# Kernel tuning notes

Measured on AMD Instinct MI355X. Metric: run time of the kernel, lower is better.

## Reference

```python
import jax, jax.numpy as jnp
import numpy as np

MAX_BITS = 64
HID = 768
B = 32768


def setup_inputs() -> dict:
    key = jax.random.key(0)
    ks = jax.random.split(key, 16)
    s = 0.02

    def w(k, shape):
        return jax.random.normal(k, shape, jnp.float32) * s

    a_bits = jnp.round(jax.random.uniform(ks[0], (B, MAX_BITS))).astype(jnp.float32)
    shift_amount = jax.random.randint(ks[1], (B,), 0, MAX_BITS).astype(jnp.int32)
    return {
        "a_bits": a_bits,
        "shift_amount": shift_amount,
        # shift_decoder: 64 -> 768 -> 768 -> 64 (weights stored [in, out])
        "Ws0": w(ks[2], (MAX_BITS, HID)), "bs0": jnp.zeros((HID,), jnp.float32),
        "Ws1": w(ks[3], (HID, HID)),      "bs1": jnp.zeros((HID,), jnp.float32),
        "Ws2": w(ks[4], (HID, MAX_BITS)), "bs2": jnp.zeros((MAX_BITS,), jnp.float32),
        # index_net: 128 -> 768 -> 768 -> 64
        "Wi0": w(ks[5], (2 * MAX_BITS, HID)), "bi0": jnp.zeros((HID,), jnp.float32),
        "Wi1": w(ks[6], (HID, HID)),          "bi1": jnp.zeros((HID,), jnp.float32),
        "Wi2": w(ks[7], (HID, MAX_BITS)),     "bi2": jnp.zeros((MAX_BITS,), jnp.float32),
        # validity_net: 128 -> 384 -> 1
        "Wv0": w(ks[8], (2 * MAX_BITS, HID // 2)), "bv0": jnp.zeros((HID // 2,), jnp.float32),
        "Wv1": w(ks[9], (HID // 2, 1)),            "bv1": jnp.zeros((1,), jnp.float32),
    }


def reference(a_bits, shift_amount, Ws0, bs0, Ws1, bs1, Ws2, bs2,
              Wi0, bi0, Wi1, bi1, Wi2, bi2, Wv0, bv0, Wv1, bv1):
    bits = a_bits.shape[1]  # == MAX_BITS == 64
    # decompose integer shift into bits: [B, bits]
    shift_bits = ((shift_amount[:, None] >> jnp.arange(bits, dtype=shift_amount.dtype)) & 1).astype(jnp.float32)
    # shift_decoder MLP -> hard one-hot of predicted shift
    h = jax.nn.relu(shift_bits @ Ws0 + bs0)
    h = jax.nn.relu(h @ Ws1 + bs1)
    shift_logits = (h @ Ws2 + bs2)[:, :bits]
    shift_soft = jax.nn.one_hot(jnp.argmax(shift_logits, axis=-1), bits, dtype=jnp.float32)  # [B, bits]
    # combined = [out_pos(one_hot(i)), shift_soft]; out_pos contribution to layer-0 is just row i of the
    # first `bits` rows of the weight, so precompute the shift_soft part once.
    base_i = shift_soft @ Wi0[bits:] + bi0   # [B, HID]
    base_v = shift_soft @ Wv0[bits:] + bv0   # [B, HID//2]

    def step(carry, i):
        h1 = jax.nn.relu(base_i + Wi0[i])                 # [B, HID]
        h2 = jax.nn.relu(h1 @ Wi1 + bi1)                  # [B, HID]
        idx_logits = (h2 @ Wi2 + bi2)[:, :bits]           # [B, bits]
        idx_soft = jax.nn.one_hot(jnp.argmax(idx_logits, axis=-1), bits, dtype=jnp.float32)
        pointed = jnp.sum(idx_soft * a_bits, axis=1)      # [B] soft gather
        hv = jax.nn.relu(base_v + Wv0[i])                 # [B, HID//2]
        valid = (hv @ Wv1 + bv1)[:, 0]                    # [B]
        return carry, pointed * jax.nn.sigmoid(valid)

    _, outs = jax.lax.scan(step, None, jnp.arange(bits))  # [bits, B]
    return outs.T                                          # [B, bits]
```

## Files before the change

kernel.cpp:

```cpp
#include <hip/hip_runtime.h>
#include <math.h>

#define HID 768
#define NB  64
#define HV  384

__device__ __forceinline__ float4 ld4(const float* p) { return *(const float4*)p; }

__global__ __launch_bounds__(256)
void dec1p_kernel(const float* __restrict__ Ws0, const float* __restrict__ bs0,
                  const float* __restrict__ Ws1, float* __restrict__ H1p) {
    __shared__ float W0s[7 * 48];
    __shared__ float As[48 * 68];
    __shared__ float Bs[48 * 68];
    const int tid = threadIdx.x;
    const int n0 = (blockIdx.x % 12) * 64;
    const int kz = blockIdx.x / 12;
    const int ks = kz * 48;

    for (int e = tid; e < 7 * 48; e += 256) {
        const int r = e / 48, c = e % 48;
        W0s[e] = (r < 6) ? Ws0[(size_t)r * HID + ks + c] : bs0[ks + c];
    }
    for (int e = tid; e < 48 * 16; e += 256) {
        const int k = e >> 4, nq = (e & 15) * 4;
        *(float4*)&Bs[k * 68 + nq] = ld4(Ws1 + (size_t)(ks + k) * HID + n0 + nq);
    }
    __syncthreads();
    for (int e = tid; e < 48 * 64; e += 256) {
        const int k = e >> 6, t = e & 63;
        float v = W0s[6 * 48 + k];
        #pragma unroll
        for (int b = 0; b < 6; ++b)
            v = fmaf((float)((t >> b) & 1), W0s[b * 48 + k], v);
        As[k * 68 + t] = fmaxf(v, 0.f);
    }
    __syncthreads();

    const int tx = tid & 15, ty = tid >> 4;
    float acc[4][4] = {};
    #pragma unroll 8
    for (int kk = 0; kk < 48; ++kk) {
        const float4 a4 = *(const float4*)&As[kk * 68 + ty * 4];
        const float4 b4 = *(const float4*)&Bs[kk * 68 + tx * 4];
        const float av[4] = {a4.x, a4.y, a4.z, a4.w};
        const float bv[4] = {b4.x, b4.y, b4.z, b4.w};
        #pragma unroll
        for (int a = 0; a < 4; ++a)
            #pragma unroll
            for (int b = 0; b < 4; ++b)
                acc[a][b] = fmaf(av[a], bv[b], acc[a][b]);
    }
    #pragma unroll
    for (int a = 0; a < 4; ++a) {
        float4 o = make_float4(acc[a][0], acc[a][1], acc[a][2], acc[a][3]);
        *(float4*)&H1p[((size_t)kz * 64 + ty * 4 + a) * HID + n0 + tx * 4] = o;
    }
}

__global__ __launch_bounds__(256)
void dec2_kernel(const float* __restrict__ H1p, const float* __restrict__ bs1,
                 const float* __restrict__ Ws2, const float* __restrict__ bs2,
                 int* __restrict__ pred) {
    __shared__ float sh[4 * HID];
    __shared__ float plp[4][4][64];
    __shared__ float lg[4][68];
    const int tid = threadIdx.x;
    const int t0 = blockIdx.x * 4;

    for (int e = tid; e < 4 * (HID / 4); e += 256) {
        const int rr = e / 192, k4 = (e % 192) * 4;
        float4 v = ld4(bs1 + k4);
        #pragma unroll
        for (int z = 0; z < 16; ++z) {
            const float4 p = ld4(H1p + ((size_t)z * 64 + t0 + rr) * HID + k4);
            v.x += p.x; v.y += p.y; v.z += p.z; v.w += p.w;
        }
        sh[rr * HID + k4 + 0] = fmaxf(v.x, 0.f);
        sh[rr * HID + k4 + 1] = fmaxf(v.y, 0.f);
        sh[rr * HID + k4 + 2] = fmaxf(v.z, 0.f);
        sh[rr * HID + k4 + 3] = fmaxf(v.w, 0.f);
    }
    __syncthreads();
    {
        const int n = tid & 63, part = tid >> 6;
        float p[4] = {0.f, 0.f, 0.f, 0.f};
        #pragma unroll 8
        for (int kk = 0; kk < 192; ++kk) {
            const int k = part * 192 + kk;
            const float w = Ws2[k * 64 + n];
            #pragma unroll
            for (int rr = 0; rr < 4; ++rr) p[rr] = fmaf(sh[rr * HID + k], w, p[rr]);
        }
        #pragma unroll
        for (int rr = 0; rr < 4; ++rr) plp[part][rr][n] = p[rr];
    }
    __syncthreads();
    {
        const int rr = tid >> 6, n = tid & 63;
        lg[rr][n] = bs2[n] + plp[0][rr][n] + plp[1][rr][n] + plp[2][rr][n] + plp[3][rr][n];
    }
    __syncthreads();
    if (tid < 4) {
        int best = 0; float bv = lg[tid][0];
        for (int n = 1; n < 64; ++n) {
            const float x = lg[tid][n];
            if (x > bv) { bv = x; best = n; }
        }
        pred[t0 + tid] = best;
    }
}

__global__ __launch_bounds__(64)
void plan_kernel(const int* __restrict__ pred, int* __restrict__ hdr) {
    const int lane = threadIdx.x;
    __shared__ int present[64];
    present[lane] = 0;
    __syncthreads();
    present[pred[lane] & 63] = 1;
    __syncthreads();
    const unsigned long long alive = __ballot(present[lane] != 0);
    const int P = __popcll(alive);
    const int rank = __popcll(alive & ((1ull << lane) - 1ull));
    if (lane == 0) hdr[0] = P;
    if (present[lane]) { hdr[1 + rank] = lane; hdr[65 + lane] = rank; }
    else hdr[65 + lane] = -1;
}

__global__ __launch_bounds__(256)
void gemmA_kernel(const float* __restrict__ Wi0, const float* __restrict__ bi0,
                  const float* __restrict__ Wi1, const int* __restrict__ hdr,
                  float* __restrict__ H2p) {
    __shared__ float As[64 * 68];
    __shared__ float Bs[64 * 40];
    const int tid = threadIdx.x;
    const int P = hdr[0];
    const int li = blockIdx.y;
    if (li >= P) return;
    const int s = hdr[1 + li];
    const int n0 = blockIdx.x * 32;
    const int z = blockIdx.z;
    const int tx = tid & 15, ty = tid >> 4;
    const float* arow = Wi0 + (size_t)(64 + s) * HID;
    float acc[4][2] = {};

    for (int kt = 0; kt < 2; ++kt) {
        const int k0 = z * 128 + kt * 64;
        #pragma unroll
        for (int pass = 0; pass < 4; ++pass) {
            const int c = pass * 256 + tid;
            const int m = c >> 4, kq = (c & 15) * 4;
            const float4 a1 = ld4(arow + k0 + kq);
            const float4 a2 = ld4(Wi0 + (size_t)m * HID + k0 + kq);
            const float4 bb = ld4(bi0 + k0 + kq);
            As[(kq + 0) * 68 + m] = fmaxf(a1.x + a2.x + bb.x, 0.f);
            As[(kq + 1) * 68 + m] = fmaxf(a1.y + a2.y + bb.y, 0.f);
            As[(kq + 2) * 68 + m] = fmaxf(a1.z + a2.z + bb.z, 0.f);
            As[(kq + 3) * 68 + m] = fmaxf(a1.w + a2.w + bb.w, 0.f);
        }
        #pragma unroll
        for (int pass = 0; pass < 2; ++pass) {
            const int c = pass * 256 + tid;
            const int k = c >> 3, nq = (c & 7) * 4;
            *(float4*)&Bs[k * 40 + nq] = ld4(Wi1 + (size_t)(k0 + k) * HID + n0 + nq);
        }
        __syncthreads();
        #pragma unroll 16
        for (int kk = 0; kk < 64; ++kk) {
            const float4 a4 = *(const float4*)&As[kk * 68 + ty * 4];
            const float2 b2 = *(const float2*)&Bs[kk * 40 + tx * 2];
            const float av[4] = {a4.x, a4.y, a4.z, a4.w};
            #pragma unroll
            for (int a = 0; a < 4; ++a) {
                acc[a][0] = fmaf(av[a], b2.x, acc[a][0]);
                acc[a][1] = fmaf(av[a], b2.y, acc[a][1]);
            }
        }
        __syncthreads();
    }
    float* dst = H2p + ((size_t)(z * 64 + li) * 64) * HID + n0 + tx * 2;
    #pragma unroll
    for (int a = 0; a < 4; ++a)
        *(float2*)(dst + (size_t)(ty * 4 + a) * HID) = make_float2(acc[a][0], acc[a][1]);
}

__global__ __launch_bounds__(256)
void gemmB_kernel(const float* __restrict__ bi1, const float* __restrict__ Wi2,
                  const int* __restrict__ hdr, const float* __restrict__ H2p,
                  float* __restrict__ PLf) {
    __shared__ float Ht[64 * 68];
    __shared__ float W2[64 * 68];
    const int tid = threadIdx.x;
    const int P = hdr[0];
    const int li = blockIdx.y;
    if (li >= P) return;
    const int bx = blockIdx.x;
    const int n0 = bx * 64;
    const size_t zstep = (size_t)64 * 64 * HID;

    for (int e = tid; e < 1024; e += 256) {
        const int m = e >> 4, nq = (e & 15) * 4;
        const float* base = H2p + ((size_t)li * 64 + m) * HID + n0 + nq;
        float4 v = ld4(base);
        #pragma unroll
        for (int z = 1; z < 6; ++z) {
            const float4 p = ld4(base + z * zstep);
            v.x += p.x; v.y += p.y; v.z += p.z; v.w += p.w;
        }
        const float4 bb = ld4(bi1 + n0 + nq);
        Ht[(nq + 0) * 68 + m] = fmaxf(v.x + bb.x, 0.f);
        Ht[(nq + 1) * 68 + m] = fmaxf(v.y + bb.y, 0.f);
        Ht[(nq + 2) * 68 + m] = fmaxf(v.z + bb.z, 0.f);
        Ht[(nq + 3) * 68 + m] = fmaxf(v.w + bb.w, 0.f);
    }
    #pragma unroll
    for (int pass = 0; pass < 4; ++pass) {
        const int c = pass * 256 + tid;
        const int cl = c >> 4, oq = (c & 15) * 4;
        *(float4*)&W2[cl * 68 + oq] = ld4(Wi2 + (size_t)(n0 + cl) * 64 + oq);
    }
    __syncthreads();
    const int tx = tid & 15, ty = tid >> 4;
    float pl_[4][4] = {};
    #pragma unroll 16
    for (int kk = 0; kk < 64; ++kk) {
        const float4 a4 = *(const float4*)&Ht[kk * 68 + ty * 4];
        const float4 b4 = *(const float4*)&W2[kk * 68 + tx * 4];
        const float av[4] = {a4.x, a4.y, a4.z, a4.w};
        const float bv[4] = {b4.x, b4.y, b4.z, b4.w};
        #pragma unroll
        for (int a = 0; a < 4; ++a)
            #pragma unroll
            for (int b = 0; b < 4; ++b)
                pl_[a][b] = fmaf(av[a], bv[b], pl_[a][b]);
    }
    #pragma unroll
    for (int a = 0; a < 4; ++a) {
        float4 o = make_float4(pl_[a][0], pl_[a][1], pl_[a][2], pl_[a][3]);
        *(float4*)&PLf[((size_t)(bx * 64 + li) * 64 + ty * 4 + a) * 64 + tx * 4] = o;
    }
}

__global__ __launch_bounds__(256)
void reduceA_kernel(const float* __restrict__ PLf, const float* __restrict__ bi2,
                    const float* __restrict__ Wv0, const float* __restrict__ bv0,
                    const float* __restrict__ Wv1, const float* __restrict__ bv1,
                    const int* __restrict__ hdr,
                    int* __restrict__ j_tab, float* __restrict__ sig_tab) {
    __shared__ float lg[16 * 68];
    const int tid = threadIdx.x;
    const int s = blockIdx.x >> 2;
    const int li = hdr[65 + s];
    if (li < 0) return;
    const int r0 = blockIdx.x * 16;
    const int rr = tid >> 4, q = tid & 15;
    const int i = (r0 & 63) + rr;
    float4 v = ld4(bi2 + q * 4);
    #pragma unroll
    for (int bx = 0; bx < 12; ++bx) {
        const float4 p = ld4(PLf + ((size_t)(bx * 64 + li) * 64 + i) * 64 + q * 4);
        v.x += p.x; v.y += p.y; v.z += p.z; v.w += p.w;
    }
    *(float4*)&lg[rr * 68 + q * 4] = v;
    __syncthreads();
    if (tid < 16) {
        int best = 0; float bv = lg[tid * 68];
        for (int n = 1; n < 64; ++n) {
            const float x = lg[tid * 68 + n];
            if (x > bv) { bv = x; best = n; }
        }
        j_tab[r0 + tid] = best;
    }
    {
        const int r = r0 + rr;
        const int ii = r & 63;
        const float* w1 = Wv0 + (size_t)(64 + s) * HV;
        const float* w2 = Wv0 + (size_t)ii * HV;
        float sum = 0.f;
        #pragma unroll 4
        for (int c = q; c < HV; c += 16) {
            const float hv = fmaxf(w1[c] + w2[c] + bv0[c], 0.f);
            sum = fmaf(hv, Wv1[c], sum);
        }
        #pragma unroll
        for (int m = 8; m >= 1; m >>= 1) sum += __shfl_xor(sum, m);
        if (q == 0) sig_tab[r] = 1.f / (1.f + expf(-(sum + bv1[0])));
    }
}

__global__ __launch_bounds__(256)
void output_kernel(const float* __restrict__ a_bits, const int* __restrict__ shift_amount,
                   const int* __restrict__ pred, const int* __restrict__ j_tab,
                   const float* __restrict__ sig_tab, float* __restrict__ out, int B) {
    const int tid = threadIdx.x;
    const int i = tid & 63;
    const int b = blockIdx.x * 4 + (tid >> 6);
    if (b >= B) return;
    const int t = shift_amount[b] & 63;
    const int s = pred[t];
    const int idx = s * 64 + i;
    const int j = j_tab[idx];
    out[(size_t)b * 64 + i] = a_bits[(size_t)b * 64 + j] * sig_tab[idx];
}

extern "C" void kernel_launch(void* const* d_in, const int* in_sizes, int n_in,
                              void* d_out, int out_size, void* d_ws, size_t ws_size,
                              hipStream_t stream) {
    const float* a_bits       = (const float*)d_in[0];
    const int*   shift_amount = (const int*)d_in[1];
    const float* Ws0 = (const float*)d_in[2];
    const float* bs0 = (const float*)d_in[3];
    const float* Ws1 = (const float*)d_in[4];
    const float* bs1 = (const float*)d_in[5];
    const float* Ws2 = (const float*)d_in[6];
    const float* bs2 = (const float*)d_in[7];
    const float* Wi0 = (const float*)d_in[8];
    const float* bi0 = (const float*)d_in[9];
    const float* Wi1 = (const float*)d_in[10];
    const float* bi1 = (const float*)d_in[11];
    const float* Wi2 = (const float*)d_in[12];
    const float* bi2 = (const float*)d_in[13];
    const float* Wv0 = (const float*)d_in[14];
    const float* bv0 = (const float*)d_in[15];
    const float* Wv1 = (const float*)d_in[16];
    const float* bv1 = (const float*)d_in[17];
    float* out = (float*)d_out;
    const int B = in_sizes[1];

    char* ws = (char*)d_ws;
    int*   pred    = (int*)ws;
    int*   j_tab   = (int*)(ws + 1024);
    float* sig_tab = (float*)(ws + 20480);
    int*   hdr     = (int*)(ws + 40960);
    float* H1p = (float*)(ws + 65536);
    float* H2p = (float*)(ws + 65536);
    float* PLf = (float*)(ws + 65536 + 75497472);

    dec1p_kernel<<<192, 256, 0, stream>>>(Ws0, bs0, Ws1, H1p);
    dec2_kernel<<<16, 256, 0, stream>>>(H1p, bs1, Ws2, bs2, pred);
    plan_kernel<<<1, 64, 0, stream>>>(pred, hdr);
    gemmA_kernel<<<dim3(24, 64, 6), 256, 0, stream>>>(Wi0, bi0, Wi1, hdr, H2p);
    gemmB_kernel<<<dim3(12, 64), 256, 0, stream>>>(bi1, Wi2, hdr, H2p, PLf);
    reduceA_kernel<<<256, 256, 0, stream>>>(PLf, bi2, Wv0, bv0, Wv1, bv1, hdr,
                                            j_tab, sig_tab);
    output_kernel<<<(B + 3) / 4, 256, 0, stream>>>(a_bits, shift_amount, pred,
                                                   j_tab, sig_tab, out, B);
}
```

Baseline: 159.5 us.

## Enlarge gemmA register tile to 8x8 and split dec2 one row per block

```diff
diff --git a/kernel.cpp b/kernel.cpp
--- a/kernel.cpp
+++ b/kernel.cpp
@@ -62,52 +62,44 @@
 void dec2_kernel(const float* __restrict__ H1p, const float* __restrict__ bs1,
                  const float* __restrict__ Ws2, const float* __restrict__ bs2,
                  int* __restrict__ pred) {
-    __shared__ float sh[4 * HID];
-    __shared__ float plp[4][4][64];
-    __shared__ float lg[4][68];
-    const int tid = threadIdx.x;
-    const int t0 = blockIdx.x * 4;
-
-    for (int e = tid; e < 4 * (HID / 4); e += 256) {
-        const int rr = e / 192, k4 = (e % 192) * 4;
+    __shared__ float sh[HID];
+    __shared__ float plp[4][64];
+    const int tid = threadIdx.x;
+    const int t = blockIdx.x;
+
+    for (int e = tid; e < HID / 4; e += 256) {
+        const int k4 = e * 4;
         float4 v = ld4(bs1 + k4);
         #pragma unroll
         for (int z = 0; z < 16; ++z) {
-            const float4 p = ld4(H1p + ((size_t)z * 64 + t0 + rr) * HID + k4);
+            const float4 p = ld4(H1p + ((size_t)z * 64 + t) * HID + k4);
             v.x += p.x; v.y += p.y; v.z += p.z; v.w += p.w;
         }
-        sh[rr * HID + k4 + 0] = fmaxf(v.x, 0.f);
-        sh[rr * HID + k4 + 1] = fmaxf(v.y, 0.f);
-        sh[rr * HID + k4 + 2] = fmaxf(v.z, 0.f);
-        sh[rr * HID + k4 + 3] = fmaxf(v.w, 0.f);
+        sh[k4 + 0] = fmaxf(v.x, 0.f);
+        sh[k4 + 1] = fmaxf(v.y, 0.f);
+        sh[k4 + 2] = fmaxf(v.z, 0.f);
+        sh[k4 + 3] = fmaxf(v.w, 0.f);
     }
     __syncthreads();
     {
         const int n = tid & 63, part = tid >> 6;
-        float p[4] = {0.f, 0.f, 0.f, 0.f};
+        float p = 0.f;
         #pragma unroll 8
         for (int kk = 0; kk < 192; ++kk) {
             const int k = part * 192 + kk;
-            const float w = Ws2[k * 64 + n];
-            #pragma unroll
-            for (int rr = 0; rr < 4; ++rr) p[rr] = fmaf(sh[rr * HID + k], w, p[rr]);
-        }
-        #pragma unroll
-        for (int rr = 0; rr < 4; ++rr) plp[part][rr][n] = p[rr];
-    }
-    __syncthreads();
-    {
-        const int rr = tid >> 6, n = tid & 63;
-        lg[rr][n] = bs2[n] + plp[0][rr][n] + plp[1][rr][n] + plp[2][rr][n] + plp[3][rr][n];
-    }
-    __syncthreads();
-    if (tid < 4) {
-        int best = 0; float bv = lg[tid][0];
+            p = fmaf(sh[k], Ws2[k * 64 + n], p);
+        }
+        plp[part][n] = p;
+    }
+    __syncthreads();
+    if (tid == 0) {
+        int best = 0;
+        float bv = bs2[0] + plp[0][0] + plp[1][0] + plp[2][0] + plp[3][0];
         for (int n = 1; n < 64; ++n) {
-            const float x = lg[tid][n];
+            const float x = bs2[n] + plp[0][n] + plp[1][n] + plp[2][n] + plp[3][n];
             if (x > bv) { bv = x; best = n; }
         }
-        pred[t0 + tid] = best;
+        pred[t] = best;
     }
 }
 
@@ -131,25 +123,25 @@
 void gemmA_kernel(const float* __restrict__ Wi0, const float* __restrict__ bi0,
                   const float* __restrict__ Wi1, const int* __restrict__ hdr,
                   float* __restrict__ H2p) {
-    __shared__ float As[64 * 68];
-    __shared__ float Bs[64 * 40];
+    __shared__ float As[32 * 68];
+    __shared__ float Bs[32 * 260];
     const int tid = threadIdx.x;
     const int P = hdr[0];
     const int li = blockIdx.y;
     if (li >= P) return;
     const int s = hdr[1 + li];
-    const int n0 = blockIdx.x * 32;
+    const int n0 = blockIdx.x * 256;
     const int z = blockIdx.z;
-    const int tx = tid & 15, ty = tid >> 4;
+    const int tx = tid & 31, ty = tid >> 5;
     const float* arow = Wi0 + (size_t)(64 + s) * HID;
-    float acc[4][2] = {};
-
-    for (int kt = 0; kt < 2; ++kt) {
-        const int k0 = z * 128 + kt * 64;
-        #pragma unroll
-        for (int pass = 0; pass < 4; ++pass) {
+    float acc[8][8] = {};
+
+    for (int kt = 0; kt < 4; ++kt) {
+        const int k0 = z * 128 + kt * 32;
+        #pragma unroll
+        for (int pass = 0; pass < 2; ++pass) {
             const int c = pass * 256 + tid;
-            const int m = c >> 4, kq = (c & 15) * 4;
+            const int m = c >> 3, kq = (c & 7) * 4;
             const float4 a1 = ld4(arow + k0 + kq);
             const float4 a2 = ld4(Wi0 + (size_t)m * HID + k0 + kq);
             const float4 bb = ld4(bi0 + k0 + kq);
@@ -159,29 +151,35 @@
             As[(kq + 3) * 68 + m] = fmaxf(a1.w + a2.w + bb.w, 0.f);
         }
         #pragma unroll
-        for (int pass = 0; pass < 2; ++pass) {
+        for (int pass = 0; pass < 8; ++pass) {
             const int c = pass * 256 + tid;
-            const int k = c >> 3, nq = (c & 7) * 4;
-            *(float4*)&Bs[k * 40 + nq] = ld4(Wi1 + (size_t)(k0 + k) * HID + n0 + nq);
+            const int k = c >> 6, nq = (c & 63) * 4;
+            *(float4*)&Bs[k * 260 + nq] = ld4(Wi1 + (size_t)(k0 + k) * HID + n0 + nq);
         }
         __syncthreads();
-        #pragma unroll 16
-        for (int kk = 0; kk < 64; ++kk) {
-            const float4 a4 = *(const float4*)&As[kk * 68 + ty * 4];
-            const float2 b2 = *(const float2*)&Bs[kk * 40 + tx * 2];
-            const float av[4] = {a4.x, a4.y, a4.z, a4.w};
+        #pragma unroll 8
+        for (int kk = 0; kk < 32; ++kk) {
+            const float4 a0 = *(const float4*)&As[kk * 68 + ty * 8];
+            const float4 a1 = *(const float4*)&As[kk * 68 + ty * 8 + 4];
+            const float4 b0 = *(const float4*)&Bs[kk * 260 + tx * 4];
+            const float4 b1 = *(const float4*)&Bs[kk * 260 + 128 + tx * 4];
+            const float av[8] = {a0.x, a0.y, a0.z, a0.w, a1.x, a1.y, a1.z, a1.w};
+            const float bv[8] = {b0.x, b0.y, b0.z, b0.w, b1.x, b1.y, b1.z, b1.w};
             #pragma unroll
-            for (int a = 0; a < 4; ++a) {
-                acc[a][0] = fmaf(av[a], b2.x, acc[a][0]);
-                acc[a][1] = fmaf(av[a], b2.y, acc[a][1]);
-            }
+            for (int a = 0; a < 8; ++a)
+                #pragma unroll
+                for (int b = 0; b < 8; ++b)
+                    acc[a][b] = fmaf(av[a], bv[b], acc[a][b]);
         }
         __syncthreads();
     }
-    float* dst = H2p + ((size_t)(z * 64 + li) * 64) * HID + n0 + tx * 2;
-    #pragma unroll
-    for (int a = 0; a < 4; ++a)
-        *(float2*)(dst + (size_t)(ty * 4 + a) * HID) = make_float2(acc[a][0], acc[a][1]);
+    float* dst = H2p + ((size_t)(z * 64 + li) * 64) * HID + n0;
+    #pragma unroll
+    for (int a = 0; a < 8; ++a) {
+        float* r = dst + (size_t)(ty * 8 + a) * HID;
+        *(float4*)(r + tx * 4)       = make_float4(acc[a][0], acc[a][1], acc[a][2], acc[a][3]);
+        *(float4*)(r + 128 + tx * 4) = make_float4(acc[a][4], acc[a][5], acc[a][6], acc[a][7]);
+    }
 }
 
 __global__ __launch_bounds__(256)
@@ -337,9 +335,9 @@
     float* PLf = (float*)(ws + 65536 + 75497472);
 
     dec1p_kernel<<<192, 256, 0, stream>>>(Ws0, bs0, Ws1, H1p);
-    dec2_kernel<<<16, 256, 0, stream>>>(H1p, bs1, Ws2, bs2, pred);
+    dec2_kernel<<<64, 256, 0, stream>>>(H1p, bs1, Ws2, bs2, pred);
     plan_kernel<<<1, 64, 0, stream>>>(pred, hdr);
-    gemmA_kernel<<<dim3(24, 64, 6), 256, 0, stream>>>(Wi0, bi0, Wi1, hdr, H2p);
+    gemmA_kernel<<<dim3(3, 64, 6), 256, 0, stream>>>(Wi0, bi0, Wi1, hdr, H2p);
     gemmB_kernel<<<dim3(12, 64), 256, 0, stream>>>(bi1, Wi2, hdr, H2p, PLf);
     reduceA_kernel<<<256, 256, 0, stream>>>(PLf, bi2, Wv0, bv0, Wv1, bv1, hdr,
                                             j_tab, sig_tab);
```

Result: slower. 168.3 us (+5.5%).

## Fuse shift decoder into one kernel and inline plan computation into consumers

Applied to the files above, without the earlier changes.

```diff
diff --git a/kernel.cpp b/kernel.cpp
--- a/kernel.cpp
+++ b/kernel.cpp
@@ -8,136 +8,97 @@
 __device__ __forceinline__ float4 ld4(const float* p) { return *(const float4*)p; }
 
 __global__ __launch_bounds__(256)
-void dec1p_kernel(const float* __restrict__ Ws0, const float* __restrict__ bs0,
-                  const float* __restrict__ Ws1, float* __restrict__ H1p) {
-    __shared__ float W0s[7 * 48];
-    __shared__ float As[48 * 68];
-    __shared__ float Bs[48 * 68];
-    const int tid = threadIdx.x;
-    const int n0 = (blockIdx.x % 12) * 64;
-    const int kz = blockIdx.x / 12;
-    const int ks = kz * 48;
-
-    for (int e = tid; e < 7 * 48; e += 256) {
-        const int r = e / 48, c = e % 48;
-        W0s[e] = (r < 6) ? Ws0[(size_t)r * HID + ks + c] : bs0[ks + c];
-    }
-    for (int e = tid; e < 48 * 16; e += 256) {
-        const int k = e >> 4, nq = (e & 15) * 4;
-        *(float4*)&Bs[k * 68 + nq] = ld4(Ws1 + (size_t)(ks + k) * HID + n0 + nq);
-    }
-    __syncthreads();
-    for (int e = tid; e < 48 * 64; e += 256) {
-        const int k = e >> 6, t = e & 63;
-        float v = W0s[6 * 48 + k];
+void dec_kernel(const float* __restrict__ Ws0, const float* __restrict__ bs0,
+                const float* __restrict__ Ws1, const float* __restrict__ bs1,
+                const float* __restrict__ Ws2, const float* __restrict__ bs2,
+                int* __restrict__ pred) {
+    __shared__ float A0s[HID];
+    __shared__ float h2s[HID];
+    __shared__ float plp[4][64];
+    const int tid = threadIdx.x;
+    const int t = blockIdx.x;
+
+    for (int k = tid; k < HID; k += 256) {
+        float v = bs0[k];
         #pragma unroll
         for (int b = 0; b < 6; ++b)
-            v = fmaf((float)((t >> b) & 1), W0s[b * 48 + k], v);
-        As[k * 68 + t] = fmaxf(v, 0.f);
-    }
-    __syncthreads();
-
-    const int tx = tid & 15, ty = tid >> 4;
-    float acc[4][4] = {};
-    #pragma unroll 8
-    for (int kk = 0; kk < 48; ++kk) {
-        const float4 a4 = *(const float4*)&As[kk * 68 + ty * 4];
-        const float4 b4 = *(const float4*)&Bs[kk * 68 + tx * 4];
-        const float av[4] = {a4.x, a4.y, a4.z, a4.w};
-        const float bv[4] = {b4.x, b4.y, b4.z, b4.w};
-        #pragma unroll
-        for (int a = 0; a < 4; ++a)
-            #pragma unroll
-            for (int b = 0; b < 4; ++b)
-                acc[a][b] = fmaf(av[a], bv[b], acc[a][b]);
-    }
-    #pragma unroll
-    for (int a = 0; a < 4; ++a) {
-        float4 o = make_float4(acc[a][0], acc[a][1], acc[a][2], acc[a][3]);
-        *(float4*)&H1p[((size_t)kz * 64 + ty * 4 + a) * HID + n0 + tx * 4] = o;
-    }
-}
-
-__global__ __launch_bounds__(256)
-void dec2_kernel(const float* __restrict__ H1p, const float* __restrict__ bs1,
-                 const float* __restrict__ Ws2, const float* __restrict__ bs2,
-                 int* __restrict__ pred) {
-    __shared__ float sh[4 * HID];
-    __shared__ float plp[4][4][64];
-    __shared__ float lg[4][68];
-    const int tid = threadIdx.x;
-    const int t0 = blockIdx.x * 4;
-
-    for (int e = tid; e < 4 * (HID / 4); e += 256) {
-        const int rr = e / 192, k4 = (e % 192) * 4;
-        float4 v = ld4(bs1 + k4);
-        #pragma unroll
+            v = fmaf((float)((t >> b) & 1), Ws0[(size_t)b * HID + k], v);
+        A0s[k] = fmaxf(v, 0.f);
+    }
+    __syncthreads();
+
+    {
+        const int n0 = tid, n1 = tid + 256, n2 = tid + 512;
+        float h0 = bs1[n0], h1 = bs1[n1], h2v = bs1[n2];
         for (int z = 0; z < 16; ++z) {
-            const float4 p = ld4(H1p + ((size_t)z * 64 + t0 + rr) * HID + k4);
-            v.x += p.x; v.y += p.y; v.z += p.z; v.w += p.w;
-        }
-        sh[rr * HID + k4 + 0] = fmaxf(v.x, 0.f);
-        sh[rr * HID + k4 + 1] = fmaxf(v.y, 0.f);
-        sh[rr * HID + k4 + 2] = fmaxf(v.z, 0.f);
-        sh[rr * HID + k4 + 3] = fmaxf(v.w, 0.f);
-    }
-    __syncthreads();
+            float p0 = 0.f, p1 = 0.f, p2 = 0.f;
+            #pragma unroll 8
+            for (int kk = 0; kk < 48; ++kk) {
+                const int k = z * 48 + kk;
+                const float a = A0s[k];
+                const float* wr = Ws1 + (size_t)k * HID;
+                p0 = fmaf(a, wr[n0], p0);
+                p1 = fmaf(a, wr[n1], p1);
+                p2 = fmaf(a, wr[n2], p2);
+            }
+            h0 += p0; h1 += p1; h2v += p2;
+        }
+        h2s[n0] = fmaxf(h0, 0.f);
+        h2s[n1] = fmaxf(h1, 0.f);
+        h2s[n2] = fmaxf(h2v, 0.f);
+    }
+    __syncthreads();
+
     {
         const int n = tid & 63, part = tid >> 6;
-        float p[4] = {0.f, 0.f, 0.f, 0.f};
+        float p = 0.f;
         #pragma unroll 8
         for (int kk = 0; kk < 192; ++kk) {
             const int k = part * 192 + kk;
-            const float w = Ws2[k * 64 + n];
-            #pragma unroll
-            for (int rr = 0; rr < 4; ++rr) p[rr] = fmaf(sh[rr * HID + k], w, p[rr]);
-        }
-        #pragma unroll
-        for (int rr = 0; rr < 4; ++rr) plp[part][rr][n] = p[rr];
-    }
-    __syncthreads();
-    {
-        const int rr = tid >> 6, n = tid & 63;
-        lg[rr][n] = bs2[n] + plp[0][rr][n] + plp[1][rr][n] + plp[2][rr][n] + plp[3][rr][n];
-    }
-    __syncthreads();
-    if (tid < 4) {
-        int best = 0; float bv = lg[tid][0];
+            p = fmaf(h2s[k], Ws2[k * 64 + n], p);
+        }
+        plp[part][n] = p;
+    }
+    __syncthreads();
+    if (tid == 0) {
+        int best = 0;
+        float bv = bs2[0] + plp[0][0] + plp[1][0] + plp[2][0] + plp[3][0];
         for (int n = 1; n < 64; ++n) {
-            const float x = lg[tid][n];
+            const float x = bs2[n] + plp[0][n] + plp[1][n] + plp[2][n] + plp[3][n];
             if (x > bv) { bv = x; best = n; }
         }
-        pred[t0 + tid] = best;
-    }
-}
-
-__global__ __launch_bounds__(64)
-void plan_kernel(const int* __restrict__ pred, int* __restrict__ hdr) {
-    const int lane = threadIdx.x;
-    __shared__ int present[64];
-    present[lane] = 0;
-    __syncthreads();
-    present[pred[lane] & 63] = 1;
-    __syncthreads();
-    const unsigned long long alive = __ballot(present[lane] != 0);
-    const int P = __popcll(alive);
-    const int rank = __popcll(alive & ((1ull << lane) - 1ull));
-    if (lane == 0) hdr[0] = P;
-    if (present[lane]) { hdr[1 + rank] = lane; hdr[65 + lane] = rank; }
-    else hdr[65 + lane] = -1;
-}
+        pred[t] = best;
+    }
+}
+
 
 __global__ __launch_bounds__(256)
 void gemmA_kernel(const float* __restrict__ Wi0, const float* __restrict__ bi0,
-                  const float* __restrict__ Wi1, const int* __restrict__ hdr,
+                  const float* __restrict__ Wi1, const int* __restrict__ pred,
                   float* __restrict__ H2p) {
     __shared__ float As[64 * 68];
     __shared__ float Bs[64 * 40];
-    const int tid = threadIdx.x;
-    const int P = hdr[0];
+    __shared__ int present[64];
+    __shared__ int shdr[65];
+    const int tid = threadIdx.x;
+
+    if (tid < 64) present[tid] = 0;
+    __syncthreads();
+    if (tid < 64) present[pred[tid] & 63] = 1;
+    __syncthreads();
+    if (tid < 64) {
+        const unsigned long long alive = __ballot(present[tid] != 0);
+        const int P = __popcll(alive);
+        const int rank = __popcll(alive & ((1ull << tid) - 1ull));
+        if (tid == 0) shdr[0] = P;
+        if (present[tid]) shdr[1 + rank] = tid;
+    }
+    __syncthreads();
+
+    const int P = shdr[0];
     const int li = blockIdx.y;
     if (li >= P) return;
-    const int s = hdr[1 + li];
+    const int s = shdr[1 + li];
     const int n0 = blockIdx.x * 32;
     const int z = blockIdx.z;
     const int tx = tid & 15, ty = tid >> 4;
@@ -186,12 +147,25 @@
 
 __global__ __launch_bounds__(256)
 void gemmB_kernel(const float* __restrict__ bi1, const float* __restrict__ Wi2,
-                  const int* __restrict__ hdr, const float* __restrict__ H2p,
+                  const int* __restrict__ pred, const float* __restrict__ H2p,
                   float* __restrict__ PLf) {
     __shared__ float Ht[64 * 68];
     __shared__ float W2[64 * 68];
-    const int tid = threadIdx.x;
-    const int P = hdr[0];
+    __shared__ int present[64];
+    __shared__ int sP;
+    const int tid = threadIdx.x;
+
+    if (tid < 64) present[tid] = 0;
+    __syncthreads();
+    if (tid < 64) present[pred[tid] & 63] = 1;
+    __syncthreads();
+    if (tid < 64) {
+        const unsigned long long alive = __ballot(present[tid] != 0);
+        if (tid == 0) sP = __popcll(alive);
+    }
+    __syncthreads();
+
+    const int P = sP;
     const int li = blockIdx.y;
     if (li >= P) return;
     const int bx = blockIdx.x;
@@ -245,12 +219,26 @@
 void reduceA_kernel(const float* __restrict__ PLf, const float* __restrict__ bi2,
                     const float* __restrict__ Wv0, const float* __restrict__ bv0,
                     const float* __restrict__ Wv1, const float* __restrict__ bv1,
-                    const int* __restrict__ hdr,
+                    const int* __restrict__ pred,
                     int* __restrict__ j_tab, float* __restrict__ sig_tab) {
     __shared__ float lg[16 * 68];
+    __shared__ int present[64];
+    __shared__ int rank_of[64];
     const int tid = threadIdx.x;
     const int s = blockIdx.x >> 2;
-    const int li = hdr[65 + s];
+
+    if (tid < 64) present[tid] = 0;
+    __syncthreads();
+    if (tid < 64) present[pred[tid] & 63] = 1;
+    __syncthreads();
+    if (tid < 64) {
+        const unsigned long long alive = __ballot(present[tid] != 0);
+        const int rank = __popcll(alive & ((1ull << tid) - 1ull));
+        rank_of[tid] = present[tid] ? rank : -1;
+    }
+    __syncthreads();
+
+    const int li = rank_of[s];
     if (li < 0) return;
     const int r0 = blockIdx.x * 16;
     const int rr = tid >> 4, q = tid & 15;
@@ -331,17 +319,13 @@
     int*   pred    = (int*)ws;
     int*   j_tab   = (int*)(ws + 1024);
     float* sig_tab = (float*)(ws + 20480);
-    int*   hdr     = (int*)(ws + 40960);
-    float* H1p = (float*)(ws + 65536);
     float* H2p = (float*)(ws + 65536);
     float* PLf = (float*)(ws + 65536 + 75497472);
 
-    dec1p_kernel<<<192, 256, 0, stream>>>(Ws0, bs0, Ws1, H1p);
-    dec2_kernel<<<16, 256, 0, stream>>>(H1p, bs1, Ws2, bs2, pred);
-    plan_kernel<<<1, 64, 0, stream>>>(pred, hdr);
-    gemmA_kernel<<<dim3(24, 64, 6), 256, 0, stream>>>(Wi0, bi0, Wi1, hdr, H2p);
-    gemmB_kernel<<<dim3(12, 64), 256, 0, stream>>>(bi1, Wi2, hdr, H2p, PLf);
-    reduceA_kernel<<<256, 256, 0, stream>>>(PLf, bi2, Wv0, bv0, Wv1, bv1, hdr,
+    dec_kernel<<<64, 256, 0, stream>>>(Ws0, bs0, Ws1, bs1, Ws2, bs2, pred);
+    gemmA_kernel<<<dim3(24, 64, 6), 256, 0, stream>>>(Wi0, bi0, Wi1, pred, H2p);
+    gemmB_kernel<<<dim3(12, 64), 256, 0, stream>>>(bi1, Wi2, pred, H2p, PLf);
+    reduceA_kernel<<<256, 256, 0, stream>>>(PLf, bi2, Wv0, bv0, Wv1, bv1, pred,
                                             j_tab, sig_tab);
     output_kernel<<<(B + 3) / 4, 256, 0, stream>>>(a_bits, shift_amount, pred,
                                                    j_tab, sig_tab, out, B);
```

Result: slower. 195.1 us (+22.3%).
